# Performance work log

Measured on AMD Instinct MI355X. Metric: run time of the kernel, lower is better.

Reference implementation:

```python
import jax, jax.numpy as jnp
import numpy as np

NUM_EXPERTS = 8
TOP_K = 2
HIDDEN = 1024
FFN = 2048  # GLU width; h_to_4h projects to 2*FFN


def setup_inputs() -> dict:
    key = jax.random.key(0)
    k0, k1, k2, k3 = jax.random.split(key, 4)
    hidden_states = jax.random.normal(k0, (2048, 4, HIDDEN), dtype=jnp.float32)
    # router: nn.Linear(hidden, num_experts, bias=False) stored as [hidden, E]
    w_router = jax.random.normal(k1, (HIDDEN, NUM_EXPERTS), dtype=jnp.float32) * 0.02
    # per-expert dense_h_to_4h weights stacked: [E, hidden, 2*FFN]
    w1 = jax.random.normal(k2, (NUM_EXPERTS, HIDDEN, 2 * FFN), dtype=jnp.float32) * 0.02
    # per-expert dense_4h_to_h weights stacked: [E, FFN, hidden]
    w2 = jax.random.normal(k3, (NUM_EXPERTS, FFN, HIDDEN), dtype=jnp.float32) * 0.02
    return {"hidden_states": hidden_states, "w_router": w_router, "w1": w1, "w2": w2}


def reference(hidden_states, w_router, w1, w2):
    s, b, n = hidden_states.shape
    x = hidden_states.reshape(-1, n)              # [T, n], T = s*b
    T = x.shape[0]
    E = w1.shape[0]

    route = x @ w_router                          # [T, E] (router math in fp32)
    vals, idx = jax.lax.top_k(route, TOP_K)       # [T, k]
    gate_k = jax.nn.softmax(vals.astype(jnp.float32), axis=1).astype(x.dtype)
    # scatter top-k gates into dense [T, E] gate matrix (zeros elsewhere);
    # top_k indices are distinct per token so .set is exact
    gates = jnp.zeros((T, E), dtype=x.dtype).at[jnp.arange(T)[:, None], idx].set(gate_k)

    out = jnp.zeros_like(x)
    for e in range(E):  # small fixed expert count; each iter is one big GEMM pair
        h = x @ w1[e]                             # [T, 2*FFN]
        a, g = jnp.split(h, 2, axis=-1)
        act = a * jax.nn.silu(g)                  # swiglu
        out = out + gates[:, e:e + 1] * (act @ w2[e])
    return out.reshape(s, b, n)
```

## Files before the change

kernel.cpp:

```cpp
#include <hip/hip_runtime.h>
#include <hip/hip_bf16.h>
#include <math.h>


#define T_TOK 8192
#define HID   1024
#define NEXP  8
#define FFN   2048
#define PADU  128
#define MAXPAD (2 * T_TOK + NEXP * PADU)
#define MT1    (MAXPAD / 128)

typedef __attribute__((ext_vector_type(4))) float f32x4;
typedef __attribute__((ext_vector_type(8))) short bf16x8;
typedef __attribute__((ext_vector_type(8))) unsigned short u16x8;

static __device__ __forceinline__ unsigned short f2bf(float f) {
  unsigned int u = __float_as_uint(f);
  u += 0x7fffu + ((u >> 16) & 1u);
  return (unsigned short)(u >> 16);
}
static __device__ __forceinline__ float bf2f(unsigned short h) {
  return __uint_as_float(((unsigned int)h) << 16);
}

#define GLDS16(gsrc, ldst)                                                  \
  __builtin_amdgcn_global_load_lds(                                        \
      (const __attribute__((address_space(1))) void*)(gsrc),               \
      (__attribute__((address_space(3))) void*)(ldst), 16, 0, 0)

__global__ __launch_bounds__(512) void k_router(
    const float* __restrict__ x, const float* __restrict__ wr,
    int* __restrict__ tok_idx, float* __restrict__ tok_gate) {
  __shared__ float wrT[8][1024];
  const int tid = threadIdx.x;
#pragma unroll
  for (int p = 0; p < 4; ++p) {
    const int idx = tid + p * 512;
    const float4 v = reinterpret_cast<const float4*>(wr)[idx];
    const int f = idx * 4;
    wrT[(f + 0) & 7][(f + 0) >> 3] = v.x;
    wrT[(f + 1) & 7][(f + 1) >> 3] = v.y;
    wrT[(f + 2) & 7][(f + 2) >> 3] = v.z;
    wrT[(f + 3) & 7][(f + 3) >> 3] = v.w;
  }
  __syncthreads();

  const int lane = tid & 63;
  const int wid  = tid >> 6;
  const int t    = blockIdx.x * 8 + wid;
  const float* xr = x + (size_t)t * HID;

  double acc[8] = {};
#pragma unroll
  for (int j = 0; j < 16; ++j) {
    const int k = lane + j * 64;
    const double xv = (double)xr[k];
#pragma unroll
    for (int e = 0; e < 8; ++e) acc[e] += xv * (double)wrT[e][k];
  }
#pragma unroll
  for (int e = 0; e < 8; ++e) {
#pragma unroll
    for (int off = 32; off > 0; off >>= 1) acc[e] += __shfl_down(acc[e], off);
  }
  if (lane == 0) {
    double v0 = -1e300, v1 = -1e300;
    int i0 = 0, i1 = 0;
#pragma unroll
    for (int e = 0; e < 8; ++e) {
      const double v = acc[e];
      if (v > v0)      { v1 = v0; i1 = i0; v0 = v; i0 = e; }
      else if (v > v1) { v1 = v; i1 = e; }
    }
    const float g0 = 1.0f / (1.0f + expf((float)(v1 - v0)));
    tok_idx[2 * t]     = i0;
    tok_idx[2 * t + 1] = i1;
    tok_gate[2 * t]     = g0;
    tok_gate[2 * t + 1] = 1.0f - g0;
  }
}

__global__ void k_count(const int* __restrict__ tok_idx, int* __restrict__ hdr) {
  __shared__ int h[8];
  const int tid = threadIdx.x;
  if (tid < 8) h[tid] = 0;
  __syncthreads();
  int c[8] = {0, 0, 0, 0, 0, 0, 0, 0};
  for (int i = tid; i < 2 * T_TOK; i += 256) {
    const int e = tok_idx[i];
#pragma unroll
    for (int q = 0; q < 8; ++q) c[q] += (e == q) ? 1 : 0;
  }
#pragma unroll
  for (int q = 0; q < 8; ++q) {
#pragma unroll
    for (int off = 32; off > 0; off >>= 1) c[q] += __shfl_down(c[q], off);
  }
  if ((tid & 63) == 0) {
#pragma unroll
    for (int q = 0; q < 8; ++q) atomicAdd(&h[q], c[q]);
  }
  __syncthreads();
  if (tid == 0) {
    int off = 0;
#pragma unroll
    for (int e = 0; e < 8; ++e) {
      hdr[e] = h[e];
      hdr[8 + e] = 0;
      hdr[16 + e] = off;
      off += (h[e] + PADU - 1) & ~(PADU - 1);
    }
    hdr[24] = off;
    hdr[25] = off;
  }
}

__global__ void k_scatter(const int* __restrict__ tok_idx, int* __restrict__ hdr,
                          int* __restrict__ bucket_tok, int* __restrict__ rowmap) {
  __shared__ int lcnt[8], lbase[8];
  const int tid = threadIdx.x;
  const int i = blockIdx.x * 256 + tid;
  const int e = tok_idx[i];
  if (tid < 8) lcnt[tid] = 0;
  __syncthreads();
  const int pos = atomicAdd(&lcnt[e], 1);
  __syncthreads();
  if (tid < 8) lbase[tid] = atomicAdd(&hdr[8 + tid], lcnt[tid]);
  __syncthreads();
  const int r = hdr[16 + e] + lbase[e] + pos;
  bucket_tok[r] = i >> 1;
  rowmap[i] = r;
}

__global__ void k_cvt_x(const float* __restrict__ x, unsigned short* __restrict__ xb) {
  const int i = blockIdx.x * 256 + threadIdx.x;
  const float4 v = reinterpret_cast<const float4*>(x)[i];
  ushort4 h;
  h.x = f2bf(v.x); h.y = f2bf(v.y); h.z = f2bf(v.z); h.w = f2bf(v.w);
  reinterpret_cast<ushort4*>(xb)[i] = h;
}

__global__ void k_cvtT(const float* __restrict__ src, unsigned short* __restrict__ dst,
                       int R, int C, int ilv) {
  const int e  = blockIdx.z;
  const int c0 = blockIdx.x * 64;
  const int r0 = blockIdx.y * 64;
  __shared__ unsigned short t[64][72];
  const int tid = threadIdx.x;
  const float* s = src + (size_t)e * R * C;
  unsigned short* d = dst + (size_t)e * R * C;
#pragma unroll
  for (int p = 0; p < 4; ++p) {
    const int idx = tid + p * 256;
    const int r  = idx >> 4;
    const int c4 = (idx & 15) << 2;
    const float4 v = *reinterpret_cast<const float4*>(s + (size_t)(r0 + r) * C + c0 + c4);
    t[c4 + 0][r] = f2bf(v.x); t[c4 + 1][r] = f2bf(v.y);
    t[c4 + 2][r] = f2bf(v.z); t[c4 + 3][r] = f2bf(v.w);
  }
  __syncthreads();
#pragma unroll
  for (int p = 0; p < 2; ++p) {
    const int idx = tid + p * 256;
    const int c  = idx >> 3;
    const int r8 = (idx & 7) << 3;
    u16x8 v;
#pragma unroll
    for (int i = 0; i < 8; ++i) v[i] = t[c][r8 + i];
    const int n = c0 + c;
    int row = n;
    if (ilv) {
      const int j = n & (FFN - 1);
      const int half = n >> 11;
      row = ((j >> 4) << 5) + (half << 4) + (j & 15);
    }
    *reinterpret_cast<u16x8*>(d + (size_t)row * R + r0 + r8) = v;
  }
}

__global__ __launch_bounds__(512, 2) void k_gemm1(
    const unsigned short* __restrict__ xb, const unsigned short* __restrict__ w1i,
    const int* __restrict__ bucket_tok, const int* __restrict__ hdr,
    unsigned short* __restrict__ act) {
  const int total = hdr[25];
  const int m0 = blockIdx.y * 128;
  if (m0 >= total) return;
  int e = 0;
#pragma unroll
  for (int q = 1; q < 8; ++q) e += (m0 >= hdr[16 + q]) ? 1 : 0;
  const int bx = blockIdx.x;
  const unsigned short* w1e = w1i + (size_t)e * 4096 * 1024;

  __shared__ __align__(16) char Lds[2 * 49152];

  const int tid  = threadIdx.x;
  const int lane = tid & 63;
  const int w    = tid >> 6;
  const int wrow = (w >> 2) * 64;
  const int wcol = (w & 3) * 64;
  const int lr   = lane & 15;
  const int qk16 = (lane >> 4) << 4;
  const int ldsw = w * 1024;

  const int srow = tid >> 3;
  const int cswz = (((tid & 7) ^ (srow & 7)) << 3);
  const int aoffA0 = bucket_tok[m0 + srow] * 1024 + cswz;
  const int aoffA1 = bucket_tok[m0 + 64 + srow] * 1024 + cswz;
  const int boffB0 = (bx * 256 + srow) * 1024 + cswz;

  f32x4 acc[4][4] = {};

#define G1_STAGE(base, kt) do {                                             \
    const unsigned short* xs = xb + (kt) * 64;                              \
    const unsigned short* ws = w1e + (kt) * 64;                             \
    GLDS16(xs + aoffA0,           Lds + (base) + ldsw);                     \
    GLDS16(xs + aoffA1,           Lds + (base) + 8192 + ldsw);              \
    GLDS16(ws + boffB0,           Lds + (base) + 16384 + ldsw);             \
    GLDS16(ws + boffB0 + 65536,   Lds + (base) + 24576 + ldsw);             \
    GLDS16(ws + boffB0 + 131072,  Lds + (base) + 32768 + ldsw);             \
    GLDS16(ws + boffB0 + 196608,  Lds + (base) + 40960 + ldsw);             \
  } while (0)

  G1_STAGE(0, 0);
  __syncthreads();

  for (int t = 0; t < 16; ++t) {
    if (t + 1 < 16) G1_STAGE(((t + 1) & 1) * 49152, t + 1);
    {
      const char* Ab = (const char*)Lds + (t & 1) * 49152;
      const char* Bb = Ab + 16384;
#pragma unroll
      for (int kk = 0; kk < 2; ++kk) {
        bf16x8 af[4], bv[4];
#pragma unroll
        for (int i = 0; i < 4; ++i) {
          const int ra = wrow + i * 16 + lr;
          af[i] = *reinterpret_cast<const bf16x8*>(Ab + ra * 128 + ((kk * 64 + qk16) ^ ((ra & 7) << 4)));
          const int rb = wcol + i * 16 + lr;
          bv[i] = *reinterpret_cast<const bf16x8*>(Bb + rb * 128 + ((kk * 64 + qk16) ^ ((rb & 7) << 4)));
        }
        __builtin_amdgcn_s_setprio(1);
#pragma unroll
        for (int mi = 0; mi < 4; ++mi)
#pragma unroll
          for (int ni = 0; ni < 4; ++ni)
            acc[mi][ni] = __builtin_amdgcn_mfma_f32_16x16x32_bf16(af[mi], bv[ni], acc[mi][ni], 0, 0, 0);
        __builtin_amdgcn_s_setprio(0);
      }
    }
    __syncthreads();
  }
#undef G1_STAGE

  const int orow = (lane >> 4) << 2;
  const int acb = bx * 128 + (wcol >> 1);
#pragma unroll
  for (int mi = 0; mi < 4; ++mi)
#pragma unroll
    for (int p = 0; p < 2; ++p) {
      const f32x4 va = acc[mi][2 * p];
      const f32x4 vg = acc[mi][2 * p + 1];
#pragma unroll
      for (int r = 0; r < 4; ++r) {
        const float g = vg[r];
        const float v = va[r] * (g / (1.0f + expf(-g)));
        const int gm = m0 + wrow + mi * 16 + orow + r;
        const int gc = acb + p * 16 + lr;
        act[(size_t)gm * FFN + gc] = f2bf(v);
      }
    }
}

__global__ __launch_bounds__(512, 4) void k_gemm2(
    const unsigned short* __restrict__ act, const unsigned short* __restrict__ w2t,
    const int* __restrict__ hdr, unsigned short* __restrict__ y) {
  const int total = hdr[25];
  const int m0 = blockIdx.y * 128;
  if (m0 >= total) return;
  int e = 0;
#pragma unroll
  for (int q = 1; q < 8; ++q) e += (m0 >= hdr[16 + q]) ? 1 : 0;
  const int n0 = blockIdx.x * 128;
  const unsigned short* w2e = w2t + (size_t)e * 1024 * 2048;

  __shared__ __align__(16) char Lds[2 * 32768];

  const int tid  = threadIdx.x;
  const int lane = tid & 63;
  const int w    = tid >> 6;
  const int wrow = (w >> 2) * 64;
  const int wcol = (w & 3) * 32;
  const int lr   = lane & 15;
  const int qk16 = (lane >> 4) << 4;
  const int ldsw = w * 1024;

  const int srow = tid >> 3;
  const int cswz = (((tid & 7) ^ (srow & 7)) << 3);
  const int aoff0 = (m0 + srow) * FFN + cswz;
  const int boff0 = (n0 + srow) * FFN + cswz;

  f32x4 acc[4][2] = {};

#define G2_STAGE(base, kt) do {                                             \
    const unsigned short* as = act + (kt) * 64;                             \
    const unsigned short* ws = w2e + (kt) * 64;                             \
    GLDS16(as + aoff0,          Lds + (base) + ldsw);                       \
    GLDS16(as + aoff0 + 131072, Lds + (base) + 8192 + ldsw);                \
    GLDS16(ws + boff0,          Lds + (base) + 16384 + ldsw);               \
    GLDS16(ws + boff0 + 131072, Lds + (base) + 24576 + ldsw);               \
  } while (0)

  G2_STAGE(0, 0);
  __syncthreads();

  for (int t = 0; t < 32; ++t) {
    if (t + 1 < 32) G2_STAGE(((t + 1) & 1) * 32768, t + 1);
    {
      const char* Ab = (const char*)Lds + (t & 1) * 32768;
      const char* Bb = Ab + 16384;
#pragma unroll
      for (int kk = 0; kk < 2; ++kk) {
        bf16x8 af[4], bv[2];
#pragma unroll
        for (int i = 0; i < 4; ++i) {
          const int ra = wrow + i * 16 + lr;
          af[i] = *reinterpret_cast<const bf16x8*>(Ab + ra * 128 + ((kk * 64 + qk16) ^ ((ra & 7) << 4)));
        }
#pragma unroll
        for (int i = 0; i < 2; ++i) {
          const int rb = wcol + i * 16 + lr;
          bv[i] = *reinterpret_cast<const bf16x8*>(Bb + rb * 128 + ((kk * 64 + qk16) ^ ((rb & 7) << 4)));
        }
        __builtin_amdgcn_s_setprio(1);
#pragma unroll
        for (int mi = 0; mi < 4; ++mi)
#pragma unroll
          for (int ni = 0; ni < 2; ++ni)
            acc[mi][ni] = __builtin_amdgcn_mfma_f32_16x16x32_bf16(af[mi], bv[ni], acc[mi][ni], 0, 0, 0);
        __builtin_amdgcn_s_setprio(0);
      }
    }
    __syncthreads();
  }
#undef G2_STAGE

  const int orow = (lane >> 4) << 2;
#pragma unroll
  for (int mi = 0; mi < 4; ++mi)
#pragma unroll
    for (int ni = 0; ni < 2; ++ni)
#pragma unroll
      for (int r = 0; r < 4; ++r) {
        const int gm = m0 + wrow + mi * 16 + orow + r;
        const int gc = n0 + wcol + ni * 16 + lr;
        y[(size_t)gm * HID + gc] = f2bf(acc[mi][ni][r]);
      }
}

__global__ void k_combine(const unsigned short* __restrict__ y,
                          const int* __restrict__ rowmap,
                          const float* __restrict__ tok_gate,
                          float* __restrict__ out) {
  const int t = blockIdx.x;
  const int c = threadIdx.x << 2;
  const int r0 = rowmap[2 * t], r1 = rowmap[2 * t + 1];
  const float g0 = tok_gate[2 * t], g1 = tok_gate[2 * t + 1];
  const ushort4 a = *reinterpret_cast<const ushort4*>(y + (size_t)r0 * HID + c);
  const ushort4 b = *reinterpret_cast<const ushort4*>(y + (size_t)r1 * HID + c);
  float4 o;
  o.x = g0 * bf2f(a.x) + g1 * bf2f(b.x);
  o.y = g0 * bf2f(a.y) + g1 * bf2f(b.y);
  o.z = g0 * bf2f(a.z) + g1 * bf2f(b.z);
  o.w = g0 * bf2f(a.w) + g1 * bf2f(b.w);
  *reinterpret_cast<float4*>(out + (size_t)t * HID + c) = o;
}

extern "C" void kernel_launch(void* const* d_in, const int* in_sizes, int n_in,
                              void* d_out, int out_size, void* d_ws, size_t ws_size,
                              hipStream_t stream) {
  const float* x  = (const float*)d_in[0];
  const float* wr = (const float*)d_in[1];
  const float* w1 = (const float*)d_in[2];
  const float* w2 = (const float*)d_in[3];
  float* out = (float*)d_out;

  char* w = (char*)d_ws;
  int*   hdr        = (int*)w;
  int*   tok_idx    = (int*)(w + 1024);
  float* tok_gate   = (float*)(w + 1024 + 65536);
  int*   rowmap     = (int*)(w + 1024 + 2 * 65536);
  int*   bucket_tok = (int*)(w + 1024 + 3 * 65536);
  const size_t R1 = 524288;
  unsigned short* xb  = (unsigned short*)(w + R1);
  unsigned short* w1i = (unsigned short*)(w + R1 + 16777216);
  unsigned short* w2t = (unsigned short*)(w + R1);
  unsigned short* yb  = (unsigned short*)(w + R1 + 33554432);
  unsigned short* act = (unsigned short*)(w + R1 + 83886080);

  hipMemsetAsync(bucket_tok, 0, MAXPAD * sizeof(int), stream);

  k_router<<<T_TOK / 8, 512, 0, stream>>>(x, wr, tok_idx, tok_gate);
  k_count<<<1, 256, 0, stream>>>(tok_idx, hdr);
  k_scatter<<<(2 * T_TOK) / 256, 256, 0, stream>>>(tok_idx, hdr, bucket_tok, rowmap);
  k_cvt_x<<<(T_TOK * HID / 4) / 256, 256, 0, stream>>>(x, xb);
  k_cvtT<<<dim3(4096 / 64, 1024 / 64, 8), 256, 0, stream>>>(w1, w1i, 1024, 4096, 1);
  k_gemm1<<<dim3(16, MT1), 512, 0, stream>>>(xb, w1i, bucket_tok, hdr, act);
  k_cvtT<<<dim3(1024 / 64, 2048 / 64, 8), 256, 0, stream>>>(w2, w2t, 2048, 1024, 0);
  k_gemm2<<<dim3(8, MT1), 512, 0, stream>>>(act, w2t, hdr, yb);
  k_combine<<<T_TOK, 256, 0, stream>>>(yb, rowmap, tok_gate, out);
}
```

Baseline: 388.5 us.

## Triple-buffer LDS in both expert GEMMs with partial vmcnt waits

Both grouped GEMM kernels move from double to triple LDS buffering. Tiles are now prefetched two k-steps ahead, and the full __syncthreads is replaced by an s_waitcnt vmcnt(N) plus s_barrier, so loads for the next-next tile can stay in flight. This is meant to hide global-to-LDS latency behind MFMA work. The cost is more LDS per block (147KB for gemm1, 96KB for gemm2), which may reduce occupancy; gemm2's launch bound drops to 2 blocks per CU accordingly.

```diff
diff --git a/kernel.cpp b/kernel.cpp
--- a/kernel.cpp
+++ b/kernel.cpp
@@ -28,6 +28,9 @@
   __builtin_amdgcn_global_load_lds(                                        \
       (const __attribute__((address_space(1))) void*)(gsrc),               \
       (__attribute__((address_space(3))) void*)(ldst), 16, 0, 0)
+
+#define SCHED_FENCE() __builtin_amdgcn_sched_barrier(0)
+#define WAIT_BAR(n) asm volatile("s_waitcnt vmcnt(" #n ")\n\ts_barrier" ::: "memory")
 
 __global__ __launch_bounds__(512) void k_router(
     const float* __restrict__ x, const float* __restrict__ wr,
@@ -192,7 +195,7 @@
   const int bx = blockIdx.x;
   const unsigned short* w1e = w1i + (size_t)e * 4096 * 1024;
 
-  __shared__ __align__(16) char Lds[2 * 49152];
+  __shared__ __align__(16) char Lds[3 * 49152];
 
   const int tid  = threadIdx.x;
   const int lane = tid & 63;
@@ -223,12 +226,19 @@
   } while (0)
 
   G1_STAGE(0, 0);
-  __syncthreads();
-
+  G1_STAGE(49152, 1);
+  SCHED_FENCE();
+  WAIT_BAR(6);
+  SCHED_FENCE();
+
+  int cur = 0, nxt2 = 2;
   for (int t = 0; t < 16; ++t) {
-    if (t + 1 < 16) G1_STAGE(((t + 1) & 1) * 49152, t + 1);
+    if (t + 2 < 16) {
+      G1_STAGE(nxt2 * 49152, t + 2);
+      SCHED_FENCE();
+    }
     {
-      const char* Ab = (const char*)Lds + (t & 1) * 49152;
+      const char* Ab = (const char*)Lds + cur * 49152;
       const char* Bb = Ab + 16384;
 #pragma unroll
       for (int kk = 0; kk < 2; ++kk) {
@@ -249,7 +259,12 @@
         __builtin_amdgcn_s_setprio(0);
       }
     }
-    __syncthreads();
+    SCHED_FENCE();
+    if (t + 2 < 16)      WAIT_BAR(6);
+    else if (t + 1 < 16) WAIT_BAR(0);
+    SCHED_FENCE();
+    cur = (cur == 2) ? 0 : (cur + 1);
+    nxt2 = (nxt2 == 2) ? 0 : (nxt2 + 1);
   }
 #undef G1_STAGE
 
@@ -272,7 +287,7 @@
     }
 }
 
-__global__ __launch_bounds__(512, 4) void k_gemm2(
+__global__ __launch_bounds__(512, 2) void k_gemm2(
     const unsigned short* __restrict__ act, const unsigned short* __restrict__ w2t,
     const int* __restrict__ hdr, unsigned short* __restrict__ y) {
   const int total = hdr[25];
@@ -284,7 +299,7 @@
   const int n0 = blockIdx.x * 128;
   const unsigned short* w2e = w2t + (size_t)e * 1024 * 2048;
 
-  __shared__ __align__(16) char Lds[2 * 32768];
+  __shared__ __align__(16) char Lds[3 * 32768];
 
   const int tid  = threadIdx.x;
   const int lane = tid & 63;
@@ -312,12 +327,19 @@
   } while (0)
 
   G2_STAGE(0, 0);
-  __syncthreads();
-
+  G2_STAGE(32768, 1);
+  SCHED_FENCE();
+  WAIT_BAR(4);
+  SCHED_FENCE();
+
+  int cur = 0, nxt2 = 2;
   for (int t = 0; t < 32; ++t) {
-    if (t + 1 < 32) G2_STAGE(((t + 1) & 1) * 32768, t + 1);
+    if (t + 2 < 32) {
+      G2_STAGE(nxt2 * 32768, t + 2);
+      SCHED_FENCE();
+    }
     {
-      const char* Ab = (const char*)Lds + (t & 1) * 32768;
+      const char* Ab = (const char*)Lds + cur * 32768;
       const char* Bb = Ab + 16384;
 #pragma unroll
       for (int kk = 0; kk < 2; ++kk) {
@@ -341,7 +363,12 @@
         __builtin_amdgcn_s_setprio(0);
       }
     }
-    __syncthreads();
+    SCHED_FENCE();
+    if (t + 2 < 32)      WAIT_BAR(4);
+    else if (t + 1 < 32) WAIT_BAR(0);
+    SCHED_FENCE();
+    cur = (cur == 2) ? 0 : (cur + 1);
+    nxt2 = (nxt2 == 2) ? 0 : (nxt2 + 1);
   }
 #undef G2_STAGE
 
```

Result: no change. 389.1 us (median of 2 runs) (+0.1%).

## Enlarge gemm1 tile to 256x256 with ping-pong staged loads; triple-buffer gemm2

Applied to the files above, without the earlier changes.

GEMM1 moves from 128x256 to 256x256 output tiles per block. Its K loop is split into four quadrant MFMA phases, with the A and B loads for future k-steps interleaved between them under explicit barriers and vmcnt waits. Expert padding grows to 256 so the bigger M tile stays inside one expert. GEMM2 gets a three-stage LDS ring with a two-step prefetch and manual waitcnt and barriers, and its occupancy hint drops to 2. The aim is more operand reuse and better hiding of load latency, at the cost of more registers, more LDS, extra padding work, and fragile hand-placed waitcnt counts.

```diff
diff --git a/kernel.cpp b/kernel.cpp
--- a/kernel.cpp
+++ b/kernel.cpp
@@ -7,9 +7,10 @@
 #define HID   1024
 #define NEXP  8
 #define FFN   2048
-#define PADU  128
+#define PADU  256
 #define MAXPAD (2 * T_TOK + NEXP * PADU)
-#define MT1    (MAXPAD / 128)
+#define MTG1   (MAXPAD / 256)
+#define MTG2   (MAXPAD / 128)
 
 typedef __attribute__((ext_vector_type(4))) float f32x4;
 typedef __attribute__((ext_vector_type(8))) short bf16x8;
@@ -28,6 +29,11 @@
   __builtin_amdgcn_global_load_lds(                                        \
       (const __attribute__((address_space(1))) void*)(gsrc),               \
       (__attribute__((address_space(3))) void*)(ldst), 16, 0, 0)
+
+#define SFENCE() __builtin_amdgcn_sched_barrier(0)
+#define BARRIER() do { SFENCE(); __builtin_amdgcn_s_barrier(); SFENCE(); } while (0)
+#define LGKM0() do { asm volatile("s_waitcnt lgkmcnt(0)" ::: "memory"); SFENCE(); } while (0)
+#define VMW(n) asm volatile("s_waitcnt vmcnt(" #n ")" ::: "memory")
 
 __global__ __launch_bounds__(512) void k_router(
     const float* __restrict__ x, const float* __restrict__ wr,
@@ -184,7 +190,7 @@
     const int* __restrict__ bucket_tok, const int* __restrict__ hdr,
     unsigned short* __restrict__ act) {
   const int total = hdr[25];
-  const int m0 = blockIdx.y * 128;
+  const int m0 = blockIdx.y * 256;
   if (m0 >= total) return;
   int e = 0;
 #pragma unroll
@@ -192,71 +198,115 @@
   const int bx = blockIdx.x;
   const unsigned short* w1e = w1i + (size_t)e * 4096 * 1024;
 
-  __shared__ __align__(16) char Lds[2 * 49152];
+  __shared__ __align__(16) char Lds[2 * 65536];
 
   const int tid  = threadIdx.x;
   const int lane = tid & 63;
   const int w    = tid >> 6;
-  const int wrow = (w >> 2) * 64;
-  const int wcol = (w & 3) * 64;
+  const int wm   = w >> 2;
+  const int wn   = w & 3;
   const int lr   = lane & 15;
   const int qk16 = (lane >> 4) << 4;
-  const int ldsw = w * 1024;
-
-  const int srow = tid >> 3;
-  const int cswz = (((tid & 7) ^ (srow & 7)) << 3);
-  const int aoffA0 = bucket_tok[m0 + srow] * 1024 + cswz;
-  const int aoffA1 = bucket_tok[m0 + 64 + srow] * 1024 + cswz;
-  const int boffB0 = (bx * 256 + srow) * 1024 + cswz;
-
-  f32x4 acc[4][4] = {};
-
-#define G1_STAGE(base, kt) do {                                             \
-    const unsigned short* xs = xb + (kt) * 64;                              \
-    const unsigned short* ws = w1e + (kt) * 64;                             \
-    GLDS16(xs + aoffA0,           Lds + (base) + ldsw);                     \
-    GLDS16(xs + aoffA1,           Lds + (base) + 8192 + ldsw);              \
-    GLDS16(ws + boffB0,           Lds + (base) + 16384 + ldsw);             \
-    GLDS16(ws + boffB0 + 65536,   Lds + (base) + 24576 + ldsw);             \
-    GLDS16(ws + boffB0 + 131072,  Lds + (base) + 32768 + ldsw);             \
-    GLDS16(ws + boffB0 + 196608,  Lds + (base) + 40960 + ldsw);             \
+  const int swz  = (lane & 7) << 4;
+  const int kb0  = qk16 ^ swz;
+  const int kb1  = (64 + qk16) ^ swz;
+
+  const int r0 = w * 16 + (lane >> 3);
+  const int cq = ((lane & 7) ^ (lane >> 3)) << 3;
+  int aoff[2][2], boff[2][2];
+#pragma unroll
+  for (int h = 0; h < 2; ++h) {
+    aoff[h][0] = bucket_tok[m0 + h * 128 + r0] * 1024 + cq;
+    aoff[h][1] = bucket_tok[m0 + h * 128 + r0 + 8] * 1024 + cq;
+    boff[h][0] = (bx * 256 + h * 128 + r0) * 1024 + cq;
+    boff[h][1] = (bx * 256 + h * 128 + r0 + 8) * 1024 + cq;
+  }
+  const int ld0 = w * 2048 + lane * 16;
+
+#define SA(dst, tt, h) do {                                                  \
+    GLDS16(xb + aoff[h][0] + (tt) * 64, (dst) + (h) * 16384 + ld0);          \
+    GLDS16(xb + aoff[h][1] + (tt) * 64, (dst) + (h) * 16384 + 1024 + ld0);   \
   } while (0)
-
-  G1_STAGE(0, 0);
-  __syncthreads();
+#define SB(dst, tt, h) do {                                                  \
+    GLDS16(w1e + boff[h][0] + (tt) * 64, (dst) + 32768 + (h) * 16384 + ld0); \
+    GLDS16(w1e + boff[h][1] + (tt) * 64, (dst) + 32768 + (h) * 16384 + 1024 + ld0); \
+  } while (0)
+
+  f32x4 acc[8][4] = {};
+  bf16x8 afq[4][2], bfr[4][2];
+
+#define RD_A(M0) do {                                                        \
+    _Pragma("unroll") for (int i = 0; i < 4; ++i) {                          \
+      const int ra = wm * 128 + ((M0) + i) * 16 + lr;                        \
+      afq[i][0] = *reinterpret_cast<const bf16x8*>(Ab + ra * 128 + kb0);     \
+      afq[i][1] = *reinterpret_cast<const bf16x8*>(Ab + ra * 128 + kb1);     \
+    } } while (0)
+#define RD_B2(N0) do {                                                       \
+    _Pragma("unroll") for (int i = 0; i < 2; ++i) {                          \
+      const int rb = wn * 64 + ((N0) + i) * 16 + lr;                         \
+      bfr[(N0) + i][0] = *reinterpret_cast<const bf16x8*>(Bb + rb * 128 + kb0); \
+      bfr[(N0) + i][1] = *reinterpret_cast<const bf16x8*>(Bb + rb * 128 + kb1); \
+    } } while (0)
+#define QUAD(M0, N0) do {                                                    \
+    __builtin_amdgcn_s_setprio(1);                                           \
+    _Pragma("unroll") for (int mi = 0; mi < 4; ++mi)                         \
+      _Pragma("unroll") for (int ni = 0; ni < 2; ++ni) {                     \
+        acc[(M0) + mi][(N0) + ni] = __builtin_amdgcn_mfma_f32_16x16x32_bf16( \
+            afq[mi][0], bfr[(N0) + ni][0], acc[(M0) + mi][(N0) + ni], 0, 0, 0); \
+        acc[(M0) + mi][(N0) + ni] = __builtin_amdgcn_mfma_f32_16x16x32_bf16( \
+            afq[mi][1], bfr[(N0) + ni][1], acc[(M0) + mi][(N0) + ni], 0, 0, 0); \
+      }                                                                      \
+    __builtin_amdgcn_s_setprio(0);                                           \
+  } while (0)
+
+  {
+    char* D0 = Lds;
+    char* D1 = Lds + 65536;
+    SB(D0, 0, 0); SB(D0, 0, 1);
+    SA(D0, 0, 0); SA(D0, 0, 1);
+    SB(D1, 1, 0); SB(D1, 1, 1);
+    SFENCE();
+    VMW(4);
+    BARRIER();
+  }
 
   for (int t = 0; t < 16; ++t) {
-    if (t + 1 < 16) G1_STAGE(((t + 1) & 1) * 49152, t + 1);
-    {
-      const char* Ab = (const char*)Lds + (t & 1) * 49152;
-      const char* Bb = Ab + 16384;
-#pragma unroll
-      for (int kk = 0; kk < 2; ++kk) {
-        bf16x8 af[4], bv[4];
-#pragma unroll
-        for (int i = 0; i < 4; ++i) {
-          const int ra = wrow + i * 16 + lr;
-          af[i] = *reinterpret_cast<const bf16x8*>(Ab + ra * 128 + ((kk * 64 + qk16) ^ ((ra & 7) << 4)));
-          const int rb = wcol + i * 16 + lr;
-          bv[i] = *reinterpret_cast<const bf16x8*>(Bb + rb * 128 + ((kk * 64 + qk16) ^ ((rb & 7) << 4)));
-        }
-        __builtin_amdgcn_s_setprio(1);
-#pragma unroll
-        for (int mi = 0; mi < 4; ++mi)
-#pragma unroll
-          for (int ni = 0; ni < 4; ++ni)
-            acc[mi][ni] = __builtin_amdgcn_mfma_f32_16x16x32_bf16(af[mi], bv[ni], acc[mi][ni], 0, 0, 0);
-        __builtin_amdgcn_s_setprio(0);
-      }
-    }
-    __syncthreads();
-  }
-#undef G1_STAGE
+    char* Ab = Lds + (t & 1) * 65536;
+    char* Bb = Ab + 32768;
+    char* Nb = Lds + ((t + 1) & 1) * 65536;
+    RD_A(0); RD_B2(0);
+    if (t < 15) SA(Nb, t + 1, 0);
+    BARRIER(); LGKM0();
+    QUAD(0, 0);
+    BARRIER();
+    RD_B2(2);
+    if (t < 15) SA(Nb, t + 1, 1);
+    BARRIER(); LGKM0();
+    QUAD(0, 2);
+    BARRIER();
+    RD_A(4);
+    if (t < 14) SB(Ab, t + 2, 0);
+    BARRIER(); LGKM0();
+    QUAD(4, 2);
+    BARRIER();
+    if (t < 14) SB(Ab, t + 2, 1);
+    BARRIER();
+    QUAD(4, 0);
+    SFENCE();
+    if (t < 14)      { VMW(4); }
+    else if (t == 14) { VMW(0); }
+    BARRIER();
+  }
+#undef SA
+#undef SB
+#undef RD_A
+#undef RD_B2
+#undef QUAD
 
   const int orow = (lane >> 4) << 2;
-  const int acb = bx * 128 + (wcol >> 1);
-#pragma unroll
-  for (int mi = 0; mi < 4; ++mi)
+  const int baseCol = bx * 128 + wn * 32;
+#pragma unroll
+  for (int mi = 0; mi < 8; ++mi) {
 #pragma unroll
     for (int p = 0; p < 2; ++p) {
       const f32x4 va = acc[mi][2 * p];
@@ -265,14 +315,15 @@
       for (int r = 0; r < 4; ++r) {
         const float g = vg[r];
         const float v = va[r] * (g / (1.0f + expf(-g)));
-        const int gm = m0 + wrow + mi * 16 + orow + r;
-        const int gc = acb + p * 16 + lr;
+        const int gm = m0 + wm * 128 + mi * 16 + orow + r;
+        const int gc = baseCol + p * 16 + lr;
         act[(size_t)gm * FFN + gc] = f2bf(v);
       }
     }
-}
-
-__global__ __launch_bounds__(512, 4) void k_gemm2(
+  }
+}
+
+__global__ __launch_bounds__(512, 2) void k_gemm2(
     const unsigned short* __restrict__ act, const unsigned short* __restrict__ w2t,
     const int* __restrict__ hdr, unsigned short* __restrict__ y) {
   const int total = hdr[25];
@@ -284,7 +335,7 @@
   const int n0 = blockIdx.x * 128;
   const unsigned short* w2e = w2t + (size_t)e * 1024 * 2048;
 
-  __shared__ __align__(16) char Lds[2 * 32768];
+  __shared__ __align__(16) char Lds[3 * 32768];
 
   const int tid  = threadIdx.x;
   const int lane = tid & 63;
@@ -312,12 +363,21 @@
   } while (0)
 
   G2_STAGE(0, 0);
-  __syncthreads();
-
+  G2_STAGE(32768, 1);
+  SFENCE();
+  asm volatile("s_waitcnt vmcnt(4)\n\ts_barrier" ::: "memory");
+  SFENCE();
+
+  int cur = 0, nxt2 = 2;
   for (int t = 0; t < 32; ++t) {
-    if (t + 1 < 32) G2_STAGE(((t + 1) & 1) * 32768, t + 1);
+    const int pre = t + 2;
+    if (pre < 32) {
+      const int pb = ((cur + 2) >= 3 ? (cur - 1) : (cur + 2)) * 32768;
+      G2_STAGE(pb, pre);
+      SFENCE();
+    }
     {
-      const char* Ab = (const char*)Lds + (t & 1) * 32768;
+      const char* Ab = (const char*)Lds + cur * 32768;
       const char* Bb = Ab + 16384;
 #pragma unroll
       for (int kk = 0; kk < 2; ++kk) {
@@ -341,7 +401,12 @@
         __builtin_amdgcn_s_setprio(0);
       }
     }
-    __syncthreads();
+    SFENCE();
+    if (pre < 32)      { asm volatile("s_waitcnt vmcnt(4)\n\ts_barrier" ::: "memory"); }
+    else if (t + 1 < 32) { asm volatile("s_waitcnt vmcnt(0)\n\ts_barrier" ::: "memory"); }
+    SFENCE();
+    cur = (cur == 2) ? 0 : (cur + 1);
+    nxt2 = (nxt2 == 2) ? 0 : (nxt2 + 1);
   }
 #undef G2_STAGE
 
@@ -405,8 +470,8 @@
   k_scatter<<<(2 * T_TOK) / 256, 256, 0, stream>>>(tok_idx, hdr, bucket_tok, rowmap);
   k_cvt_x<<<(T_TOK * HID / 4) / 256, 256, 0, stream>>>(x, xb);
   k_cvtT<<<dim3(4096 / 64, 1024 / 64, 8), 256, 0, stream>>>(w1, w1i, 1024, 4096, 1);
-  k_gemm1<<<dim3(16, MT1), 512, 0, stream>>>(xb, w1i, bucket_tok, hdr, act);
+  k_gemm1<<<dim3(16, MTG1), 512, 0, stream>>>(xb, w1i, bucket_tok, hdr, act);
   k_cvtT<<<dim3(1024 / 64, 2048 / 64, 8), 256, 0, stream>>>(w2, w2t, 2048, 1024, 0);
-  k_gemm2<<<dim3(8, MT1), 512, 0, stream>>>(act, w2t, hdr, yb);
+  k_gemm2<<<dim3(8, MTG2), 512, 0, stream>>>(act, w2t, hdr, yb);
   k_combine<<<T_TOK, 256, 0, stream>>>(yb, rowmap, tok_gate, out);
 }
```

After: 390.5 us. About the same (+0.5%).
